# Performance work log

Hardware: AMD Instinct MI355X
Metric: run time of the kernel (lower is better)

## Reference

```python
import jax, jax.numpy as jnp
import numpy as np

D = 1024
H = 16
DH = D // H  # 64
FF_H = 4096
EPS = 1e-5


def layernorm(x, gamma, beta):
    mu = jnp.mean(x, axis=-1, keepdims=True)
    var = jnp.var(x, axis=-1, keepdims=True)
    return (x - mu) * jax.lax.rsqrt(var + EPS) * gamma + beta


def setup_inputs() -> dict:
    key = jax.random.key(0)
    ks = jax.random.split(key, 12)
    B, S = 2, 2048
    q = jax.random.normal(ks[0], (B, S, D), dtype=jnp.float32)
    k = jax.random.normal(ks[1], (B, S, D), dtype=jnp.float32)
    v = jax.random.normal(ks[2], (B, S, D), dtype=jnp.float32)
    time_lengths = jax.random.randint(ks[3], (B,), 0, S)
    mask = jnp.zeros((1, 1, S, S), dtype=jnp.float32)
    sc = 0.02
    Wq = jax.random.normal(ks[4], (D, D), dtype=jnp.float32) * sc
    Wk = jax.random.normal(ks[5], (D, D), dtype=jnp.float32) * sc
    Wv = jax.random.normal(ks[6], (D, D), dtype=jnp.float32) * sc
    Wd = jax.random.normal(ks[7], (D, D), dtype=jnp.float32) * sc
    W1 = jax.random.normal(ks[8], (D, FF_H), dtype=jnp.float32) * sc
    b1 = jnp.zeros((FF_H,), dtype=jnp.float32)
    W2 = jax.random.normal(ks[9], (FF_H, D), dtype=jnp.float32) * sc
    b2 = jnp.zeros((D,), dtype=jnp.float32)
    g1 = jnp.ones((D,), dtype=jnp.float32)
    be1 = jnp.zeros((D,), dtype=jnp.float32)
    g2 = jnp.ones((D,), dtype=jnp.float32)
    be2 = jnp.zeros((D,), dtype=jnp.float32)
    return {"q": q, "k": k, "v": v, "time_lengths": time_lengths, "mask": mask,
            "Wq": Wq, "Wk": Wk, "Wv": Wv, "Wd": Wd,
            "W1": W1, "b1": b1, "W2": W2, "b2": b2,
            "g1": g1, "be1": be1, "g2": g2, "be2": be2}


def reference(q, k, v, time_lengths, mask, Wq, Wk, Wv, Wd, W1, b1, W2, b2, g1, be1, g2, be2):
    B, S, _ = q.shape
    scale = jnp.sqrt(jnp.float32(DH))
    # project and split heads: [B,H,S,DH]
    qh = (q @ Wq).reshape(B, S, H, DH).transpose(0, 2, 1, 3)
    kh = (k @ Wk).reshape(B, S, H, DH).transpose(0, 2, 1, 3)
    vh = (v @ Wv).reshape(B, S, H, DH).transpose(0, 2, 1, 3)
    score = jnp.einsum('bhqd,bhkd->bhqk', qh, kh) / scale + mask
    attn = jax.nn.softmax(score, axis=-1)
    z = jnp.einsum('bhqk,bhkd->bhqd', attn, vh)
    z = z.transpose(0, 2, 1, 3).reshape(B, S, D)
    z = z @ Wd
    # Add & LayerNorm 1 (note: original applies LN to attn out, then adds q)
    x = layernorm(z, g1, be1) + q
    # FF (dropout is identity in eval)
    ff = jax.nn.relu(x @ W1 + b1) @ W2 + b2
    return layernorm(ff + x, g2, be2)
```

## Files before the change

### kernel.cpp

```cpp
#include <hip/hip_runtime.h>
#include <hip/hip_bf16.h>


#define SEQ 2048
#define DM  1024
#define LNEPS 1e-5f

typedef __attribute__((ext_vector_type(8))) short bf16x8;
typedef __attribute__((ext_vector_type(4))) float f32x4;

#define GAS __attribute__((address_space(1)))
#define LAS __attribute__((address_space(3)))

static __device__ __forceinline__ void gl_lds16(const unsigned short* g, unsigned short* l) {
    __builtin_amdgcn_global_load_lds((const GAS void*)g, (LAS void*)l, 16, 0, 0);
}

static __device__ __forceinline__ unsigned short f2bf(float f) {
    unsigned u = __builtin_bit_cast(unsigned, f);
    u += 0x7fffu + ((u >> 16) & 1u);
    return (unsigned short)(u >> 16);
}

static __device__ __forceinline__ unsigned cvt_pk_bf16(float lo, float hi) {
    unsigned r;
    asm("v_cvt_pk_bf16_f32 %0, %1, %2" : "=v"(r) : "v"(lo), "v"(hi));
    return r;
}

__global__ __launch_bounds__(256) void gemm_bf16(
    const unsigned short* __restrict__ A, const unsigned short* __restrict__ Bt,
    float* __restrict__ Cf, unsigned short* __restrict__ Cb,
    unsigned short* __restrict__ CbT,
    int M, int N, int Klen, int lda, int ldb,
    size_t sA, size_t sB, size_t sC,
    const float* __restrict__ bias, int ep)
{
    __shared__ unsigned short As[2][128 * 32];
    __shared__ unsigned short Bs[2][128 * 32];

    const int t = threadIdx.x, lane = t & 63, w = t >> 6;
    const int wm = w >> 1, wn = w & 1;
    const int m0 = blockIdx.y * 128, n0 = blockIdx.x * 128;
    A  += (size_t)blockIdx.z * sA;
    Bt += (size_t)blockIdx.z * sB;
    const size_t cbase = (size_t)blockIdx.z * sC;
    const int l15 = lane & 15, l16 = lane >> 4;
    const int ar = lane >> 2, ac = (lane & 3) * 8;

    f32x4 acc[4][4];
    #pragma unroll
    for (int i = 0; i < 4; i++)
        #pragma unroll
        for (int j = 0; j < 4; j++)
            acc[i][j] = (f32x4){0.f, 0.f, 0.f, 0.f};

    auto stage = [&](int buf, int k0) {
        #pragma unroll
        for (int i = 0; i < 2; i++) {
            const int rg = w * 2 + i;
            gl_lds16(&A [(size_t)(m0 + rg * 16 + ar) * lda + k0 + ac], &As[buf][rg * 512]);
            gl_lds16(&Bt[(size_t)(n0 + rg * 16 + ar) * ldb + k0 + ac], &Bs[buf][rg * 512]);
        }
    };
    auto compute = [&](int buf) {
        bf16x8 af[4], bfr[4];
        #pragma unroll
        for (int i = 0; i < 4; i++) {
            af[i]  = *(const bf16x8*)&As[buf][(wm * 64 + i * 16 + l15) * 32 + l16 * 8];
            bfr[i] = *(const bf16x8*)&Bs[buf][(wn * 64 + i * 16 + l15) * 32 + l16 * 8];
        }
        #pragma unroll
        for (int mi = 0; mi < 4; mi++)
            #pragma unroll
            for (int ni = 0; ni < 4; ni++)
                acc[mi][ni] = __builtin_amdgcn_mfma_f32_16x16x32_bf16(
                    af[mi], bfr[ni], acc[mi][ni], 0, 0, 0);
    };

    stage(0, 0);
    __syncthreads();
    int k0 = 0;
    for (; k0 + 32 < Klen; k0 += 32) {
        const int cur = (k0 >> 5) & 1;
        stage(cur ^ 1, k0 + 32);
        compute(cur);
        __syncthreads();
    }
    compute((k0 >> 5) & 1);

    if (CbT && blockIdx.z == 2) {
        #pragma unroll
        for (int ni = 0; ni < 4; ni++) {
            const int col = n0 + wn * 64 + ni * 16 + l15;
            const int hh = col >> 6, d = col & 63;
            #pragma unroll
            for (int mi = 0; mi < 4; mi++) {
                const int row = m0 + wm * 64 + mi * 16 + l16 * 4;
                const int bb = row >> 11, s = row & 2047;
                ushort4 o;
                o.x = f2bf(acc[mi][ni][0]); o.y = f2bf(acc[mi][ni][1]);
                o.z = f2bf(acc[mi][ni][2]); o.w = f2bf(acc[mi][ni][3]);
                *(ushort4*)&CbT[((size_t)((bb * 16 + hh) * 64 + d)) * SEQ + s] = o;
            }
        }
        return;
    }

    #pragma unroll
    for (int ni = 0; ni < 4; ni++) {
        const int col = n0 + wn * 64 + ni * 16 + l15;
        const float bv = (ep && blockIdx.z == 0) ? bias[col] : 0.f;
        #pragma unroll
        for (int mi = 0; mi < 4; mi++) {
            #pragma unroll
            for (int r = 0; r < 4; r++) {
                const int row = m0 + wm * 64 + mi * 16 + l16 * 4 + r;
                float vv = acc[mi][ni][r] + bv;
                if (ep == 2) vv = fmaxf(vv, 0.f);
                if (Cf) Cf[cbase + (size_t)row * N + col] = vv;
                else    Cb[cbase + (size_t)row * N + col] = f2bf(vv);
            }
        }
    }
}

__global__ __launch_bounds__(256) void attn_mfma(
    const unsigned short* __restrict__ qh, const unsigned short* __restrict__ kh,
    const unsigned short* __restrict__ vhT, const float* __restrict__ mask,
    unsigned short* __restrict__ z)
{
    __shared__ unsigned short Ks0[64 * 64];
    __shared__ unsigned short Ks1[64 * 64];
    __shared__ unsigned short Vst[64 * 64];
    __shared__ unsigned short Ps[64 * 72];

    const int t = threadIdx.x, lane = t & 63, w = t >> 6;
    const int bid = blockIdx.x;
    const int qt = bid >> 5, h = bid & 15, b = (bid >> 4) & 1;
    const int q0 = qt * 64, qr = w * 16;
    const int l15 = lane & 15, l16 = lane >> 4;

    const int lr = lane >> 3;
    const int gc = ((lane & 7) ^ lr) * 8;

    const size_t qbase = (size_t)(b * SEQ + q0) * DM + h * 64;
    const size_t kbase = (size_t)(b * SEQ) * DM + h * 64;
    const size_t vbase = (size_t)((b * 16 + h) * 64) * SEQ;

    #pragma unroll
    for (int i = 0; i < 2; i++) {
        const int rg = w * 2 + i;
        gl_lds16(&qh[qbase + (size_t)(rg * 8 + lr) * DM + gc], &Ks1[rg * 512]);
        gl_lds16(&kh[kbase + (size_t)(rg * 8 + lr) * DM + gc], &Ks0[rg * 512]);
    }
    __syncthreads();

    const int sw0 = ((l16    ) ^ (l15 & 7)) * 8;
    const int sw1 = ((l16 + 4) ^ (l15 & 7)) * 8;
    const bf16x8 bQ0 = *(const bf16x8*)&Ks1[(qr + l15) * 64 + sw0];
    const bf16x8 bQ1 = *(const bf16x8*)&Ks1[(qr + l15) * 64 + sw1];
    __syncthreads();

    const float* mrow = mask + (size_t)(q0 + qr + l15) * SEQ;

    float m_i = -1e30f, l_i = 0.f;
    f32x4 o4[4];
    #pragma unroll
    for (int mi = 0; mi < 4; mi++) o4[mi] = (f32x4){0.f, 0.f, 0.f, 0.f};

    for (int kt = 0; kt < SEQ / 64; kt++) {
        const int k0 = kt * 64;
        const int kn = ((kt + 1) & (SEQ / 64 - 1)) * 64;
        unsigned short* Kcur = (kt & 1) ? Ks1 : Ks0;
        unsigned short* Knxt = (kt & 1) ? Ks0 : Ks1;

        __builtin_amdgcn_s_barrier();

        float4 mv[4];
        #pragma unroll
        for (int ki = 0; ki < 4; ki++)
            mv[ki] = *(const float4*)&mrow[k0 + ki * 16 + l16 * 4];

        #pragma unroll
        for (int i = 0; i < 2; i++) {
            const int rg = w * 2 + i;
            gl_lds16(&vhT[vbase + (size_t)(rg * 8 + lr) * SEQ + k0 + gc], &Vst[rg * 512]);
        }
        __builtin_amdgcn_sched_barrier(0);
        #pragma unroll
        for (int i = 0; i < 2; i++) {
            const int rg = w * 2 + i;
            gl_lds16(&kh[kbase + (size_t)(kn + rg * 8 + lr) * DM + gc], &Knxt[rg * 512]);
        }

        asm volatile("s_waitcnt vmcnt(8)" ::: "memory");
        __builtin_amdgcn_s_barrier();
        __builtin_amdgcn_sched_barrier(0);

        f32x4 s4[4];
        __builtin_amdgcn_s_setprio(1);
        #pragma unroll
        for (int ki = 0; ki < 4; ki++) {
            const int r = ki * 16 + l15;
            const bf16x8 aK0 = *(const bf16x8*)&Kcur[r * 64 + sw0];
            const bf16x8 aK1 = *(const bf16x8*)&Kcur[r * 64 + sw1];
            f32x4 a0 = (f32x4){0.f, 0.f, 0.f, 0.f};
            a0 = __builtin_amdgcn_mfma_f32_16x16x32_bf16(aK0, bQ0, a0, 0, 0, 0);
            s4[ki] = __builtin_amdgcn_mfma_f32_16x16x32_bf16(aK1, bQ1, a0, 0, 0, 0);
        }
        __builtin_amdgcn_s_setprio(0);

        float sv[16];
        #pragma unroll
        for (int ki = 0; ki < 4; ki++) {
            sv[ki * 4 + 0] = s4[ki][0] * 0.125f + mv[ki].x;
            sv[ki * 4 + 1] = s4[ki][1] * 0.125f + mv[ki].y;
            sv[ki * 4 + 2] = s4[ki][2] * 0.125f + mv[ki].z;
            sv[ki * 4 + 3] = s4[ki][3] * 0.125f + mv[ki].w;
        }

        float rm = fmaxf(sv[0], sv[1]);
        #pragma unroll
        for (int i = 2; i < 16; i += 2) rm = fmaxf(fmaxf(rm, sv[i]), sv[i + 1]);
        rm = fmaxf(rm, __shfl_xor(rm, 16));
        rm = fmaxf(rm, __shfl_xor(rm, 32));

        const bool skip = __all(rm <= m_i + 8.f);
        float mnew = m_i, alpha = 1.f;
        if (!skip) { mnew = fmaxf(m_i, rm); alpha = __expf(m_i - mnew); }

        float ps = 0.f;
        #pragma unroll
        for (int ki = 0; ki < 4; ki++) {
            const float p0 = __expf(sv[ki * 4 + 0] - mnew);
            const float p1 = __expf(sv[ki * 4 + 1] - mnew);
            const float p2 = __expf(sv[ki * 4 + 2] - mnew);
            const float p3 = __expf(sv[ki * 4 + 3] - mnew);
            ps += (p0 + p1) + (p2 + p3);
            uint2 pk;
            pk.x = cvt_pk_bf16(p0, p1);
            pk.y = cvt_pk_bf16(p2, p3);
            *(uint2*)&Ps[(qr + l15) * 72 + ki * 16 + l16 * 4] = pk;
        }
        ps += __shfl_xor(ps, 16);
        ps += __shfl_xor(ps, 32);
        if (!skip) {
            m_i = mnew;
            l_i = l_i * alpha + ps;
            #pragma unroll
            for (int mi = 0; mi < 4; mi++)
                #pragma unroll
                for (int r = 0; r < 4; r++) o4[mi][r] *= alpha;
        } else {
            l_i += ps;
        }

        asm volatile("s_waitcnt vmcnt(2)" ::: "memory");
        __builtin_amdgcn_s_barrier();
        __builtin_amdgcn_sched_barrier(0);

        const bf16x8 bP0 = *(const bf16x8*)&Ps[(qr + l15) * 72 + l16 * 8];
        const bf16x8 bP1 = *(const bf16x8*)&Ps[(qr + l15) * 72 + 32 + l16 * 8];
        __builtin_amdgcn_s_setprio(1);
        #pragma unroll
        for (int mi = 0; mi < 4; mi++) {
            const int r = mi * 16 + l15;
            const bf16x8 aV0 = *(const bf16x8*)&Vst[r * 64 + sw0];
            const bf16x8 aV1 = *(const bf16x8*)&Vst[r * 64 + sw1];
            o4[mi] = __builtin_amdgcn_mfma_f32_16x16x32_bf16(aV0, bP0, o4[mi], 0, 0, 0);
            o4[mi] = __builtin_amdgcn_mfma_f32_16x16x32_bf16(aV1, bP1, o4[mi], 0, 0, 0);
        }
        __builtin_amdgcn_s_setprio(0);
    }

    asm volatile("s_waitcnt vmcnt(0)" ::: "memory");

    const float inv = 1.f / l_i;
    #pragma unroll
    for (int mi = 0; mi < 4; mi++) {
        const float a0 = o4[mi][0] * inv, a1 = o4[mi][1] * inv;
        const float a2 = o4[mi][2] * inv, a3 = o4[mi][3] * inv;
        uint2 ov;
        ov.x = cvt_pk_bf16(a0, a1);
        ov.y = cvt_pk_bf16(a2, a3);
        *(uint2*)&z[(size_t)(b * SEQ + q0 + qr + l15) * DM + h * 64 + mi * 16 + l16 * 4] = ov;
    }
}

__global__ __launch_bounds__(256) void prep(
    const float* __restrict__ q, const float* __restrict__ k, const float* __restrict__ v,
    unsigned short* __restrict__ qb,
    const float* __restrict__ Wq, const float* __restrict__ Wk,
    const float* __restrict__ Wv, const float* __restrict__ Wd,
    const float* __restrict__ W1, const float* __restrict__ W2,
    unsigned short* __restrict__ Wqt, unsigned short* __restrict__ Wdt,
    unsigned short* __restrict__ W1t, unsigned short* __restrict__ W2t)
{
    const int z = blockIdx.z, t = threadIdx.x;
    const int flat = blockIdx.y * 64 + blockIdx.x;

    if (z < 3) {
        const float* src = z == 0 ? q : (z == 1 ? k : v);
        unsigned short* dst = qb + (size_t)z * ((size_t)SEQ * 2 * DM);
        const size_t base = (size_t)flat * 4096 + t * 4;
        #pragma unroll
        for (int i = 0; i < 4; i++) {
            const float4 w4 = *(const float4*)&src[base + i * 1024];
            ushort4 o; o.x = f2bf(w4.x); o.y = f2bf(w4.y); o.z = f2bf(w4.z); o.w = f2bf(w4.w);
            *(ushort4*)&dst[base + i * 1024] = o;
        }
        return;
    }

    __shared__ float ts[64][65];
    const float* W; unsigned short* Wt; int K, N, n0, k0;
    if (z < 7) {
        if (flat >= 256) return;
        W  = z == 3 ? Wq : z == 4 ? Wk : (z == 5 ? Wv : Wd);
        Wt = z == 3 ? Wqt : z == 4 ? Wqt + 1024 * 1024
           : z == 5 ? Wqt + 2 * 1024 * 1024 : Wdt;
        K = 1024; N = 1024;
        n0 = (flat & 15) * 64; k0 = (flat >> 4) * 64;
    } else if (z == 7) {
        W = W1; Wt = W1t; K = 1024; N = 4096;
        n0 = blockIdx.x * 64; k0 = blockIdx.y * 64;
    } else {
        W = W2; Wt = W2t; K = 4096; N = 1024;
        n0 = (flat & 15) * 64; k0 = (flat >> 4) * 64;
    }

    const int r = t >> 4, c4 = (t & 15) * 4;
    #pragma unroll
    for (int i = 0; i < 4; i++) {
        const float4 v4 = *(const float4*)&W[(size_t)(k0 + r + i * 16) * N + n0 + c4];
        ts[r + i * 16][c4 + 0] = v4.x; ts[r + i * 16][c4 + 1] = v4.y;
        ts[r + i * 16][c4 + 2] = v4.z; ts[r + i * 16][c4 + 3] = v4.w;
    }
    __syncthreads();
    #pragma unroll
    for (int i = 0; i < 4; i++) {
        const int n = r + i * 16;
        ushort4 o;
        o.x = f2bf(ts[c4 + 0][n]); o.y = f2bf(ts[c4 + 1][n]);
        o.z = f2bf(ts[c4 + 2][n]); o.w = f2bf(ts[c4 + 3][n]);
        *(ushort4*)&Wt[(size_t)(n0 + n) * K + k0 + c4] = o;
    }
}

__global__ __launch_bounds__(256) void ln_res(
    const float* __restrict__ a, const float* __restrict__ a2,
    const float* __restrict__ r,
    const float* __restrict__ g, const float* __restrict__ be,
    float* __restrict__ out, unsigned short* __restrict__ outb, int mode)
{
    __shared__ float redls[8];
    const int row = blockIdx.x, t = threadIdx.x;
    const size_t base = (size_t)row * DM;

    float vals[4], s = 0.f, sq = 0.f;
    #pragma unroll
    for (int i = 0; i < 4; i++) {
        const int c = t + 256 * i;
        float x = a[base + c];
        if (a2) x += a2[base + c];
        if (mode == 1) x += r[base + c];
        vals[i] = x; s += x; sq += x * x;
    }
    #pragma unroll
    for (int off = 32; off > 0; off >>= 1) { s += __shfl_down(s, off); sq += __shfl_down(sq, off); }
    if ((t & 63) == 0) { redls[t >> 6] = s; redls[4 + (t >> 6)] = sq; }
    __syncthreads();
    s  = redls[0] + redls[1] + redls[2] + redls[3];
    sq = redls[4] + redls[5] + redls[6] + redls[7];

    const float mu  = s * (1.f / 1024.f);
    const float var = sq * (1.f / 1024.f) - mu * mu;
    const float rs  = rsqrtf(var + LNEPS);
    #pragma unroll
    for (int i = 0; i < 4; i++) {
        const int c = t + 256 * i;
        float y = (vals[i] - mu) * rs * g[c] + be[c];
        if (mode == 0) y += r[base + c];
        out[base + c] = y;
        if (outb) outb[base + c] = f2bf(y);
    }
}

extern "C" void kernel_launch(void* const* d_in, const int* in_sizes, int n_in,
                              void* d_out, int out_size, void* d_ws, size_t ws_size,
                              hipStream_t stream)
{
    const float* q    = (const float*)d_in[0];
    const float* k    = (const float*)d_in[1];
    const float* v    = (const float*)d_in[2];
    const float* mask = (const float*)d_in[4];
    const float* Wq   = (const float*)d_in[5];
    const float* Wk   = (const float*)d_in[6];
    const float* Wv   = (const float*)d_in[7];
    const float* Wd   = (const float*)d_in[8];
    const float* W1   = (const float*)d_in[9];
    const float* b1   = (const float*)d_in[10];
    const float* W2   = (const float*)d_in[11];
    const float* b2   = (const float*)d_in[12];
    const float* g1   = (const float*)d_in[13];
    const float* be1  = (const float*)d_in[14];
    const float* g2   = (const float*)d_in[15];
    const float* be2  = (const float*)d_in[16];
    float* out = (float*)d_out;

    char* WS = (char*)d_ws;
    const size_t MiB = 1u << 20;
    const size_t ND  = (size_t)4096 * 1024;

    unsigned short* qb  = (unsigned short*)(WS + 0);
    unsigned short* zb  = (unsigned short*)(WS + 8 * MiB);
    unsigned short* xb  = (unsigned short*)(WS + 16 * MiB);
    unsigned short* Wqt = (unsigned short*)(WS + 24 * MiB);
    unsigned short* Wdt = (unsigned short*)(WS + 30 * MiB);
    unsigned short* W1t = (unsigned short*)(WS + 32 * MiB);
    unsigned short* W2t = (unsigned short*)(WS + 40 * MiB);
    unsigned short* qh  = (unsigned short*)(WS + 48 * MiB);
    unsigned short* vhT = (unsigned short*)(WS + 64 * MiB);
    float*          zd0 = (float*)(WS + 48 * MiB);
    float*          zd1 = (float*)(WS + 64 * MiB);
    float*          x   = (float*)(WS + 80 * MiB);
    unsigned short* h1  = (unsigned short*)(WS + 96 * MiB);
    float*          y0  = (float*)(WS + 48 * MiB);
    float*          y1  = (float*)(WS + 64 * MiB);

    unsigned short* kh = qh + ND;

    const dim3 blk(256);

    prep<<<dim3(64, 16, 9), blk, 0, stream>>>(q, k, v, qb, Wq, Wk, Wv, Wd, W1, W2,
                                              Wqt, Wdt, W1t, W2t);

    gemm_bf16<<<dim3(8, 32, 3), blk, 0, stream>>>(qb, Wqt, nullptr, qh, vhT,
        4096, 1024, 1024, 1024, 1024, ND, (size_t)1024 * 1024, ND, nullptr, 0);

    attn_mfma<<<dim3(1024), blk, 0, stream>>>(qh, kh, vhT, mask, zb);

    gemm_bf16<<<dim3(8, 32, 2), blk, 0, stream>>>(zb, Wdt, zd0, nullptr, nullptr,
        4096, 1024, 512, 1024, 1024, 512, 512, ND, nullptr, 0);

    ln_res<<<dim3(4096), blk, 0, stream>>>(zd0, zd1, q, g1, be1, x, xb, 0);

    gemm_bf16<<<dim3(32, 32, 1), blk, 0, stream>>>(xb, W1t, nullptr, h1, nullptr,
        4096, 4096, 1024, 1024, 1024, 0, 0, 0, b1, 2);
    gemm_bf16<<<dim3(8, 32, 2), blk, 0, stream>>>(h1, W2t, y0, nullptr, nullptr,
        4096, 1024, 2048, 4096, 4096, 2048, 2048, ND, b2, 1);

    ln_res<<<dim3(4096), blk, 0, stream>>>(y0, y1, x, g2, be2, out, nullptr, 1);
}
```

Baseline: 477.3 us.

## Add XCD-aware tile swizzle to GEMMs and split FFN2 K four ways

The GEMM kernel now takes a flat 1D grid and remaps block IDs so that blocks landing on the same XCD get neighbouring output tiles, improving L2 reuse of the A and B panels. The FFN down-projection switches from 2-way to 4-way split-K, writing four fp32 partials into free workspace regions. A zskip index remap steps over the slot that overlaps the W2 weights. The final LayerNorm now sums all four partials. The extra partials add memory traffic in the LayerNorm and rely on careful workspace aliasing in exchange for more blocks to fill the machine.

```diff
diff --git a/kernel.cpp b/kernel.cpp
--- a/kernel.cpp
+++ b/kernel.cpp
@@ -34,17 +34,23 @@
     unsigned short* __restrict__ CbT,
     int M, int N, int Klen, int lda, int ldb,
     size_t sA, size_t sB, size_t sC,
-    const float* __restrict__ bias, int ep)
+    const float* __restrict__ bias, int ep, int lgn, int zskip)
 {
     __shared__ unsigned short As[2][128 * 32];
     __shared__ unsigned short Bs[2][128 * 32];
 
     const int t = threadIdx.x, lane = t & 63, w = t >> 6;
     const int wm = w >> 1, wn = w & 1;
-    const int m0 = blockIdx.y * 128, n0 = blockIdx.x * 128;
+
+    const int nwg = gridDim.x;
+    const int sw = (blockIdx.x & 7) * (nwg >> 3) + (blockIdx.x >> 3);
+    const int n0 = (sw & ((1 << lgn) - 1)) * 128;
+    const int m0 = (sw >> lgn) * 128;
+
     A  += (size_t)blockIdx.z * sA;
     Bt += (size_t)blockIdx.z * sB;
-    const size_t cbase = (size_t)blockIdx.z * sC;
+    int zi = blockIdx.z; if (zskip && zi >= 2) zi++;
+    const size_t cbase = (size_t)zi * sC;
     const int l15 = lane & 15, l16 = lane >> 4;
     const int ar = lane >> 2, ac = (lane & 3) * 8;
 
@@ -350,6 +356,7 @@
 
 __global__ __launch_bounds__(256) void ln_res(
     const float* __restrict__ a, const float* __restrict__ a2,
+    const float* __restrict__ a3, const float* __restrict__ a4,
     const float* __restrict__ r,
     const float* __restrict__ g, const float* __restrict__ be,
     float* __restrict__ out, unsigned short* __restrict__ outb, int mode)
@@ -364,6 +371,8 @@
         const int c = t + 256 * i;
         float x = a[base + c];
         if (a2) x += a2[base + c];
+        if (a3) x += a3[base + c];
+        if (a4) x += a4[base + c];
         if (mode == 1) x += r[base + c];
         vals[i] = x; s += x; sq += x * x;
     }
@@ -426,8 +435,10 @@
     float*          zd1 = (float*)(WS + 64 * MiB);
     float*          x   = (float*)(WS + 80 * MiB);
     unsigned short* h1  = (unsigned short*)(WS + 96 * MiB);
-    float*          y0  = (float*)(WS + 48 * MiB);
-    float*          y1  = (float*)(WS + 64 * MiB);
+    float*          y0  = (float*)(WS + 0);
+    float*          y1  = (float*)(WS + 16 * MiB);
+    float*          y2  = (float*)(WS + 48 * MiB);
+    float*          y3  = (float*)(WS + 64 * MiB);
 
     unsigned short* kh = qh + ND;
 
@@ -436,20 +447,21 @@
     prep<<<dim3(64, 16, 9), blk, 0, stream>>>(q, k, v, qb, Wq, Wk, Wv, Wd, W1, W2,
                                               Wqt, Wdt, W1t, W2t);
 
-    gemm_bf16<<<dim3(8, 32, 3), blk, 0, stream>>>(qb, Wqt, nullptr, qh, vhT,
-        4096, 1024, 1024, 1024, 1024, ND, (size_t)1024 * 1024, ND, nullptr, 0);
+    gemm_bf16<<<dim3(256, 1, 3), blk, 0, stream>>>(qb, Wqt, nullptr, qh, vhT,
+        4096, 1024, 1024, 1024, 1024, ND, (size_t)1024 * 1024, ND, nullptr, 0, 3, 0);
 
     attn_mfma<<<dim3(1024), blk, 0, stream>>>(qh, kh, vhT, mask, zb);
 
-    gemm_bf16<<<dim3(8, 32, 2), blk, 0, stream>>>(zb, Wdt, zd0, nullptr, nullptr,
-        4096, 1024, 512, 1024, 1024, 512, 512, ND, nullptr, 0);
-
-    ln_res<<<dim3(4096), blk, 0, stream>>>(zd0, zd1, q, g1, be1, x, xb, 0);
-
-    gemm_bf16<<<dim3(32, 32, 1), blk, 0, stream>>>(xb, W1t, nullptr, h1, nullptr,
-        4096, 4096, 1024, 1024, 1024, 0, 0, 0, b1, 2);
-    gemm_bf16<<<dim3(8, 32, 2), blk, 0, stream>>>(h1, W2t, y0, nullptr, nullptr,
-        4096, 1024, 2048, 4096, 4096, 2048, 2048, ND, b2, 1);
-
-    ln_res<<<dim3(4096), blk, 0, stream>>>(y0, y1, x, g2, be2, out, nullptr, 1);
-}
+    gemm_bf16<<<dim3(256, 1, 2), blk, 0, stream>>>(zb, Wdt, zd0, nullptr, nullptr,
+        4096, 1024, 512, 1024, 1024, 512, 512, ND, nullptr, 0, 3, 0);
+
+    ln_res<<<dim3(4096), blk, 0, stream>>>(zd0, zd1, nullptr, nullptr, q,
+                                           g1, be1, x, xb, 0);
+
+    gemm_bf16<<<dim3(1024, 1, 1), blk, 0, stream>>>(xb, W1t, nullptr, h1, nullptr,
+        4096, 4096, 1024, 1024, 1024, 0, 0, 0, b1, 2, 5, 0);
+    gemm_bf16<<<dim3(256, 1, 4), blk, 0, stream>>>(h1, W2t, y0, nullptr, nullptr,
+        4096, 1024, 1024, 4096, 4096, 1024, 1024, ND, b2, 1, 3, 1);
+
+    ln_res<<<dim3(4096), blk, 0, stream>>>(y0, y1, y2, y3, x, g2, be2, out, nullptr, 1);
+}
```

New measurement: 481.9 us. About the same (+1.0%).
